# Performance work log

Hardware: AMD Instinct MI355X
Metric: run time of the kernel (lower is better)

The kernel has to match this reference:

```python
import jax, jax.numpy as jnp
import numpy as np

VEC_SIZE = 256
N_VECS = 8
N_CHOICES = 2048
BATCH = 2048
EPS = 1e-6
NAND_BIAS = 3.0


def setup_inputs() -> dict:
    key = jax.random.key(0)
    k1, k2 = jax.random.split(key)
    query = jax.random.normal(k1, (BATCH, N_VECS * VEC_SIZE), dtype=jnp.float32)
    weight = jax.random.normal(k2, (N_CHOICES, VEC_SIZE * N_VECS), dtype=jnp.float32)
    # init code overwrites the randn nand_weight with ones + nand_bias
    nand_weight = jnp.full((N_CHOICES, N_VECS), 1.0 + NAND_BIAS, dtype=jnp.float32)
    return {"query": query, "weight": weight, "nand_weight": nand_weight}


def reference(query, weight, nand_weight):
    # [B, n_vecs, vec_size] and [C, n_vecs, vec_size]
    q = query.reshape(-1, N_VECS, VEC_SIZE)
    w = weight.reshape(-1, N_VECS, VEC_SIZE)
    # torch.cosine_similarity clamps each norm to eps
    qn = q / jnp.maximum(jnp.linalg.norm(q, axis=-1, keepdims=True), EPS)
    wn = w / jnp.maximum(jnp.linalg.norm(w, axis=-1, keepdims=True), EPS)
    # broadcast cosine sim expressed as batched matmul: [B, C, n_vecs]
    cos_sim = jnp.einsum('bnd,cnd->bcn', qn, wn)
    cos_sim = jax.nn.leaky_relu(cos_sim)  # slope 0.01, matches F.leaky_relu default
    nw = jax.nn.sigmoid(nand_weight)[None]  # [1, C, n_vecs]
    interpolated = nw * cos_sim + (1.0 - nw) * (1.0 - cos_sim)
    return jnp.prod(interpolated, axis=2)  # [B, C]
```

## Files before the change

### kernel.cpp

```cpp
#include <hip/hip_runtime.h>
#include <math.h>
#include <stdint.h>

#define BATCH    2048
#define NCHOICES 2048
#define NV       8
#define VS       256
#define KTOT     2048

typedef unsigned short u16;
typedef __attribute__((ext_vector_type(8))) short    bf16x8;
typedef __attribute__((ext_vector_type(8))) u16      u16x8;
typedef __attribute__((ext_vector_type(4))) float    f32x4;

__device__ __forceinline__ u16 f2bf_rne(float x) {
    unsigned u = __float_as_uint(x);
    return (u16)((u + 0x7FFFu + ((u >> 16) & 1u)) >> 16);
}

__global__ __launch_bounds__(256) void prep_convert(
    const float* __restrict__ Q, const float* __restrict__ W,
    const float* __restrict__ NWT,
    u16* __restrict__ Qh, u16* __restrict__ Ql,
    u16* __restrict__ Wh, u16* __restrict__ Wl,
    float* __restrict__ rq, float* __restrict__ rw, float* __restrict__ snw)
{
    const int row = blockIdx.x;
    const int t   = threadIdx.x;
    const int n   = t >> 5;
    const int l   = t & 31;

    const float* src; u16 *dh, *dl; float* dst;
    if (row < BATCH) {
        src = Q + (size_t)row * KTOT;
        dh = Qh + (size_t)row * KTOT; dl = Ql + (size_t)row * KTOT;
        dst = rq + (size_t)row * NV;
    } else {
        src = W + (size_t)(row - BATCH) * KTOT;
        dh = Wh + (size_t)(row - BATCH) * KTOT; dl = Wl + (size_t)(row - BATCH) * KTOT;
        dst = rw + (size_t)(row - BATCH) * NV;
    }

    const int idx = n * VS + l * 8;
    float4 x0 = *(const float4*)(src + idx);
    float4 x1 = *(const float4*)(src + idx + 4);
    float xs[8] = {x0.x, x0.y, x0.z, x0.w, x1.x, x1.y, x1.z, x1.w};

    u16x8 hv, lv;
    float s = 0.0f;
    #pragma unroll
    for (int j = 0; j < 8; ++j) {
        u16 h = f2bf_rne(xs[j]);
        float hf = __uint_as_float(((unsigned)h) << 16);
        hv[j] = h;
        lv[j] = f2bf_rne(xs[j] - hf);
        s = fmaf(xs[j], xs[j], s);
    }
    *(u16x8*)(dh + idx) = hv;
    *(u16x8*)(dl + idx) = lv;

    #pragma unroll
    for (int m = 1; m < 32; m <<= 1) s += __shfl_xor(s, m, 64);
    if (l == 0) dst[n] = 1.0f / fmaxf(sqrtf(s), 1e-6f);

    if (row >= BATCH && t < NV) {
        const int c = row - BATCH;
        float x = NWT[(size_t)c * NV + t];
        snw[(size_t)c * NV + t] = 1.0f / (1.0f + expf(-x));
    }
}

__device__ __forceinline__ void gload16(const void* g, void* l) {
    __builtin_amdgcn_global_load_lds(
        (__attribute__((address_space(1))) void*)(uintptr_t)g,
        (__attribute__((address_space(3))) void*)(uint32_t)(uintptr_t)l,
        16, 0, 0);
}

__device__ __forceinline__ bf16x8 lds_rd16(const u16* p) {
    f32x4 r;
    asm volatile("ds_read_b128 %0, %1"
                 : "=v"(r)
                 : "v"((uint32_t)(uintptr_t)p));
    return __builtin_bit_cast(bf16x8, r);
}

#define SWZ(R, G) ((R) * 32 + ((((G) ^ (((R) >> 1) & 3))) << 3))

__global__ __launch_bounds__(512, 2) void nand_mfma8(
    const u16* __restrict__ Qh, const u16* __restrict__ Ql,
    const u16* __restrict__ Wh, const u16* __restrict__ Wl,
    const float* __restrict__ rq, const float* __restrict__ rw,
    const float* __restrict__ snw, float* __restrict__ part)
{
    __shared__ __align__(16) u16 L[3][24576];

    const int tid  = threadIdx.x;
    const int lane = tid & 63;
    const int wave = tid >> 6;
    const int wr   = (wave >> 2) * 64;
    const int wc   = (wave & 3) * 64;
    const int bm0  = blockIdx.y * 128;
    const int bn0  = blockIdx.x * 256;
    const int z    = blockIdx.z;
    const int kb   = z * 1024;

    const int fr = lane & 15;
    const int gi = lane >> 4;
    const int ri = gi * 4;

    const int gr  = tid >> 2;
    const int gg  = tid & 3;
    const int gsw = (gg ^ ((gr >> 1) & 3)) * 8;

    const u16* sAh  = Qh + (size_t)(bm0 + gr) * KTOT + kb + gsw;
    const u16* sAl  = Ql + (size_t)(bm0 + gr) * KTOT + kb + gsw;
    const u16* sB0h = Wh + (size_t)(bn0 + gr) * KTOT + kb + gsw;
    const u16* sB1h = Wh + (size_t)(bn0 + 128 + gr) * KTOT + kb + gsw;
    const u16* sB0l = Wl + (size_t)(bn0 + gr) * KTOT + kb + gsw;
    const u16* sB1l = Wl + (size_t)(bn0 + 128 + gr) * KTOT + kb + gsw;

    #define STAGE_A(B, T)  do { u16* Lb_ = &L[B][0];                        \
        gload16(sAh  + (T) * 32, Lb_ + tid * 8);                            \
        gload16(sAl  + (T) * 32, Lb_ + 4096  + tid * 8); } while (0)
    #define STAGE_BH(B, T) do { u16* Lb_ = &L[B][0];                        \
        gload16(sB0h + (T) * 32, Lb_ + 8192  + tid * 8);                    \
        gload16(sB1h + (T) * 32, Lb_ + 12288 + tid * 8); } while (0)
    #define STAGE_BL(B, T) do { u16* Lb_ = &L[B][0];                        \
        gload16(sB0l + (T) * 32, Lb_ + 16384 + tid * 8);                    \
        gload16(sB1l + (T) * 32, Lb_ + 20480 + tid * 8); } while (0)

    #define RD_A(M) do {                                                    \
        ah[M] = lds_rd16(Lb + SWZ(wr + (M) * 16 + fr, gi));                 \
        al[M] = lds_rd16(Lb + 4096 + SWZ(wr + (M) * 16 + fr, gi)); } while (0)
    #define RD_B(N) do {                                                    \
        bh[N] = lds_rd16(Lb + 8192  + SWZ(wc + (N) * 16 + fr, gi));         \
        bl[N] = lds_rd16(Lb + 16384 + SWZ(wc + (N) * 16 + fr, gi)); } while (0)

    #define MM(M, N) do {                                                   \
        acc[M][N] = __builtin_amdgcn_mfma_f32_16x16x32_bf16(ah[M], bh[N], acc[M][N], 0, 0, 0); \
        acc[M][N] = __builtin_amdgcn_mfma_f32_16x16x32_bf16(ah[M], bl[N], acc[M][N], 0, 0, 0); \
        acc[M][N] = __builtin_amdgcn_mfma_f32_16x16x32_bf16(al[M], bh[N], acc[M][N], 0, 0, 0); } while (0)

    #define WAIT_LGKM0() do {                                               \
        asm volatile("s_waitcnt lgkmcnt(0)");                               \
        __builtin_amdgcn_sched_barrier(0); } while (0)

    f32x4 prod[4][4];
    #pragma unroll
    for (int m = 0; m < 4; ++m)
        #pragma unroll
        for (int n = 0; n < 4; ++n) prod[m][n] = (f32x4){1.f, 1.f, 1.f, 1.f};

    STAGE_A(0, 0); STAGE_BH(0, 0); STAGE_BL(0, 0);
    STAGE_A(1, 1); STAGE_BH(1, 1); STAGE_BL(1, 1);
    asm volatile("s_waitcnt vmcnt(6)");
    __builtin_amdgcn_s_barrier();

    int buf = 0, bufp = 2;

    #pragma unroll 1
    for (int cc = 0; cc < 4; ++cc) {
        const int chunk = z * 4 + cc;

        float rqv[4][4];
        #pragma unroll
        for (int m = 0; m < 4; ++m)
            #pragma unroll
            for (int i = 0; i < 4; ++i)
                rqv[m][i] = rq[(size_t)(bm0 + wr + m * 16 + ri + i) * NV + chunk];
        float rwv[4], vv[4], uu[4];
        #pragma unroll
        for (int n = 0; n < 4; ++n) {
            const int col = bn0 + wc + n * 16 + fr;
            rwv[n] = rw[(size_t)col * NV + chunk];
            float s = snw[(size_t)col * NV + chunk];
            vv[n] = 2.0f * s - 1.0f;
            uu[n] = 1.0f - s;
        }

        f32x4 acc[4][4];
        #pragma unroll
        for (int m = 0; m < 4; ++m)
            #pragma unroll
            for (int n = 0; n < 4; ++n) acc[m][n] = (f32x4){0.f, 0.f, 0.f, 0.f};

        #pragma unroll 1
        for (int t8 = 0; t8 < 8; ++t8) {
            const int t = cc * 8 + t8;
            const u16* Lb = &L[buf][0];
            const bool pf = (t + 2) < 32;

            bf16x8 ah[4], al[4], bh[4], bl[4];

            RD_A(0); RD_A(1); RD_B(0); RD_B(1);
            if (pf) STAGE_A(bufp, t + 2);
            __builtin_amdgcn_s_barrier();
            WAIT_LGKM0();
            __builtin_amdgcn_s_setprio(1);
            MM(0, 0); MM(0, 1); MM(1, 0); MM(1, 1);
            __builtin_amdgcn_s_setprio(0);
            __builtin_amdgcn_s_barrier();

            RD_B(2); RD_B(3);
            if (pf) STAGE_BH(bufp, t + 2);
            __builtin_amdgcn_s_barrier();
            WAIT_LGKM0();
            __builtin_amdgcn_s_setprio(1);
            MM(0, 2); MM(0, 3); MM(1, 2); MM(1, 3);
            __builtin_amdgcn_s_setprio(0);
            __builtin_amdgcn_s_barrier();

            RD_A(2); RD_A(3);
            if (pf) STAGE_BL(bufp, t + 2);
            __builtin_amdgcn_s_barrier();
            WAIT_LGKM0();
            __builtin_amdgcn_s_setprio(1);
            MM(2, 2); MM(2, 3); MM(3, 2); MM(3, 3);
            __builtin_amdgcn_s_setprio(0);
            __builtin_amdgcn_s_barrier();

            __builtin_amdgcn_s_setprio(1);
            MM(2, 0); MM(2, 1); MM(3, 0); MM(3, 1);
            __builtin_amdgcn_s_setprio(0);

            if (t < 30) {
                asm volatile("s_waitcnt vmcnt(6)");
                __builtin_amdgcn_s_barrier();
            } else if (t == 30) {
                asm volatile("s_waitcnt vmcnt(0)");
                __builtin_amdgcn_s_barrier();
            }
            buf  = (buf  == 2) ? 0 : buf  + 1;
            bufp = (bufp == 2) ? 0 : bufp + 1;
        }

        #pragma unroll
        for (int m = 0; m < 4; ++m)
            #pragma unroll
            for (int i = 0; i < 4; ++i)
                #pragma unroll
                for (int n = 0; n < 4; ++n) {
                    float cosv = acc[m][n][i] * rqv[m][i] * rwv[n];
                    float Lk = fmaxf(cosv, 0.01f * cosv);
                    prod[m][n][i] *= fmaf(Lk, vv[n], uu[n]);
                }
    }

    float* P = part + (size_t)z * BATCH * NCHOICES;
    #pragma unroll
    for (int m = 0; m < 4; ++m)
        #pragma unroll
        for (int i = 0; i < 4; ++i) {
            const int row = bm0 + wr + m * 16 + ri + i;
            float* pr = P + (size_t)row * NCHOICES + bn0 + wc + fr;
            #pragma unroll
            for (int n = 0; n < 4; ++n) pr[n * 16] = prod[m][n][i];
        }

    #undef STAGE_A
    #undef STAGE_BH
    #undef STAGE_BL
    #undef RD_A
    #undef RD_B
    #undef MM
    #undef WAIT_LGKM0
}

__global__ __launch_bounds__(256) void combine_kernel(
    const float* __restrict__ p, float* __restrict__ out)
{
    const size_t NN = (size_t)BATCH * NCHOICES;
    size_t i = ((size_t)blockIdx.x * 256 + threadIdx.x) * 4;
    float4 a = *(const float4*)(p + i);
    float4 b = *(const float4*)(p + NN + i);
    float4 o;
    o.x = a.x * b.x;
    o.y = a.y * b.y;
    o.z = a.z * b.z;
    o.w = a.w * b.w;
    *(float4*)(out + i) = o;
}

__global__ __launch_bounds__(256) void prep_kernel(
    const float* __restrict__ Q, const float* __restrict__ W,
    const float* __restrict__ NWT,
    float* __restrict__ rq, float* __restrict__ rw, float* __restrict__ snw)
{
    const int row = blockIdx.x;
    const int t   = threadIdx.x;
    const int n   = t >> 5;
    const int l   = t & 31;

    const float* src; float* dst;
    if (row < BATCH) { src = Q + (size_t)row * KTOT; dst = rq + (size_t)row * NV; }
    else { src = W + (size_t)(row - BATCH) * KTOT; dst = rw + (size_t)(row - BATCH) * NV; }

    const float* v = src + n * VS + l * 8;
    float4 a = *(const float4*)(v);
    float4 b = *(const float4*)(v + 4);
    float s = a.x*a.x + a.y*a.y + a.z*a.z + a.w*a.w
            + b.x*b.x + b.y*b.y + b.z*b.z + b.w*b.w;
    #pragma unroll
    for (int m = 1; m < 32; m <<= 1) s += __shfl_xor(s, m, 64);
    if (l == 0) dst[n] = 1.0f / fmaxf(sqrtf(s), 1e-6f);
    if (row >= BATCH && t < NV) {
        const int c = row - BATCH;
        float x = NWT[(size_t)c * NV + t];
        snw[(size_t)c * NV + t] = 1.0f / (1.0f + expf(-x));
    }
}

__global__ __launch_bounds__(256, 2) void nand_gemm(
    const float* __restrict__ Q, const float* __restrict__ W,
    const float* __restrict__ rq, const float* __restrict__ rw,
    const float* __restrict__ snw, float* __restrict__ out)
{
    __shared__ __align__(16) float As[16][128 + 4];
    __shared__ __align__(16) float Bs[16][128 + 4];
    __shared__ __align__(16) float rqs[128];
    __shared__ __align__(16) float rws[128];
    __shared__ __align__(16) float sns[128];

    const int tid = threadIdx.x;
    const int tx  = tid & 15;
    const int ty  = tid >> 4;
    const int bm0 = blockIdx.y * 128;
    const int bn0 = blockIdx.x * 128;
    const int lr  = tid >> 2;
    const int lk  = (tid & 3) * 4;

    float prod[8][8];
    #pragma unroll
    for (int i = 0; i < 8; ++i)
        #pragma unroll
        for (int j = 0; j < 8; ++j) prod[i][j] = 1.0f;

    for (int n = 0; n < NV; ++n) {
        float acc[8][8];
        #pragma unroll
        for (int i = 0; i < 8; ++i)
            #pragma unroll
            for (int j = 0; j < 8; ++j) acc[i][j] = 0.0f;

        #pragma unroll 1
        for (int kt = 0; kt < VS / 16; ++kt) {
            const int k0 = n * VS + kt * 16;
            __syncthreads();
            {
                const float* qrow = Q + (size_t)(bm0 + lr) * KTOT + k0 + lk;
                float4 a0 = *(const float4*)(qrow);
                float4 a1 = *(const float4*)(qrow + (size_t)64 * KTOT);
                As[lk + 0][lr] = a0.x; As[lk + 1][lr] = a0.y;
                As[lk + 2][lr] = a0.z; As[lk + 3][lr] = a0.w;
                As[lk + 0][64 + lr] = a1.x; As[lk + 1][64 + lr] = a1.y;
                As[lk + 2][64 + lr] = a1.z; As[lk + 3][64 + lr] = a1.w;

                const float* wrow = W + (size_t)(bn0 + lr) * KTOT + k0 + lk;
                float4 b0 = *(const float4*)(wrow);
                float4 b1 = *(const float4*)(wrow + (size_t)64 * KTOT);
                Bs[lk + 0][lr] = b0.x; Bs[lk + 1][lr] = b0.y;
                Bs[lk + 2][lr] = b0.z; Bs[lk + 3][lr] = b0.w;
                Bs[lk + 0][64 + lr] = b1.x; Bs[lk + 1][64 + lr] = b1.y;
                Bs[lk + 2][64 + lr] = b1.z; Bs[lk + 3][64 + lr] = b1.w;
            }
            if (kt == 0) {
                for (int i = tid; i < 3 * 128; i += 256) {
                    if (i < 128)      rqs[i]       = rq[(size_t)(bm0 + i) * NV + n];
                    else if (i < 256) rws[i - 128] = rw[(size_t)(bn0 + i - 128) * NV + n];
                    else              sns[i - 256] = snw[(size_t)(bn0 + i - 256) * NV + n];
                }
            }
            __syncthreads();

            #pragma unroll
            for (int kk = 0; kk < 16; ++kk) {
                float4 a0 = *(const float4*)&As[kk][ty * 4];
                float4 a1 = *(const float4*)&As[kk][64 + ty * 4];
                float4 b0 = *(const float4*)&Bs[kk][tx * 4];
                float4 b1 = *(const float4*)&Bs[kk][64 + tx * 4];
                float ar[8] = {a0.x, a0.y, a0.z, a0.w, a1.x, a1.y, a1.z, a1.w};
                float br[8] = {b0.x, b0.y, b0.z, b0.w, b1.x, b1.y, b1.z, b1.w};
                #pragma unroll
                for (int i = 0; i < 8; ++i)
                    #pragma unroll
                    for (int j = 0; j < 8; ++j)
                        acc[i][j] = fmaf(ar[i], br[j], acc[i][j]);
            }
        }

        float rwv[8], uu[8], vv[8];
        #pragma unroll
        for (int j = 0; j < 8; ++j) {
            int cc = (j < 4) ? (tx * 4 + j) : (64 + tx * 4 + (j - 4));
            rwv[j] = rws[cc];
            float s = sns[cc];
            uu[j] = 1.0f - s;
            vv[j] = 2.0f * s - 1.0f;
        }
        #pragma unroll
        for (int i = 0; i < 8; ++i) {
            int r = (i < 4) ? (ty * 4 + i) : (64 + ty * 4 + (i - 4));
            float rqv = rqs[r];
            #pragma unroll
            for (int j = 0; j < 8; ++j) {
                float cosv = acc[i][j] * rqv * rwv[j];
                float Lk = fmaxf(cosv, 0.01f * cosv);
                prod[i][j] *= fmaf(Lk, vv[j], uu[j]);
            }
        }
    }

    #pragma unroll
    for (int i = 0; i < 8; ++i) {
        int r = (i < 4) ? (ty * 4 + i) : (64 + ty * 4 + (i - 4));
        float* orow = out + (size_t)(bm0 + r) * NCHOICES + bn0;
        float4 o0 = {prod[i][0], prod[i][1], prod[i][2], prod[i][3]};
        float4 o1 = {prod[i][4], prod[i][5], prod[i][6], prod[i][7]};
        *(float4*)(orow + tx * 4)      = o0;
        *(float4*)(orow + 64 + tx * 4) = o1;
    }
}

extern "C" void kernel_launch(void* const* d_in, const int* in_sizes, int n_in,
                              void* d_out, int out_size, void* d_ws, size_t ws_size,
                              hipStream_t stream)
{
    const float* Q   = (const float*)d_in[0];
    const float* W   = (const float*)d_in[1];
    const float* NWT = (const float*)d_in[2];
    float* out = (float*)d_out;

    char* w = (char*)d_ws;
    float* rq  = (float*)w; w += (size_t)BATCH    * NV * 4;
    float* rwn = (float*)w; w += (size_t)NCHOICES * NV * 4;
    float* snw = (float*)w; w += (size_t)NCHOICES * NV * 4;
    u16* Qh = (u16*)w; w += (size_t)BATCH * KTOT * 2;
    u16* Ql = (u16*)w; w += (size_t)BATCH * KTOT * 2;
    u16* Wh = (u16*)w; w += (size_t)NCHOICES * KTOT * 2;
    u16* Wl = (u16*)w; w += (size_t)NCHOICES * KTOT * 2;
    float* part = (float*)w; w += (size_t)2 * BATCH * NCHOICES * 4;
    const size_t needed = (size_t)(w - (char*)d_ws);

    if (ws_size >= needed) {
        prep_convert<<<BATCH + NCHOICES, 256, 0, stream>>>(
            Q, W, NWT, Qh, Ql, Wh, Wl, rq, rwn, snw);
        dim3 grid(NCHOICES / 256, BATCH / 128, 2);
        nand_mfma8<<<grid, 512, 0, stream>>>(Qh, Ql, Wh, Wl, rq, rwn, snw, part);
        combine_kernel<<<(BATCH * NCHOICES / 4) / 256, 256, 0, stream>>>(part, out);
    } else {
        prep_kernel<<<BATCH + NCHOICES, 256, 0, stream>>>(Q, W, NWT, rq, rwn, snw);
        dim3 grid(NCHOICES / 128, BATCH / 128);
        nand_gemm<<<grid, 256, 0, stream>>>(Q, W, rq, rwn, snw, out);
    }
}
```

Before: 84.51 us.

## Replace 8-wave triple-buffered GEMM with 4-wave double-buffered 128x128 tile kernel

The split-bf16 MFMA kernel goes from a 128x256 tile with 8 waves and a three-stage LDS ring to a 128x128 tile with 4 waves and a simple double buffer. Each step prefetches the next tile, reads all fragments, and issues all MFMAs in one block, with one barrier per step. The goal is to cut the many per-step barriers and the interleaving of phases, and to raise block count for better occupancy. In exchange, per-block data reuse drops (more global/L2 traffic per flop) and latency hiding is shallower.

```diff
diff --git a/kernel.cpp b/kernel.cpp
--- a/kernel.cpp
+++ b/kernel.cpp
@@ -87,21 +87,21 @@
 
 #define SWZ(R, G) ((R) * 32 + ((((G) ^ (((R) >> 1) & 3))) << 3))
 
-__global__ __launch_bounds__(512, 2) void nand_mfma8(
+__global__ __launch_bounds__(256, 2) void nand_mfma2b(
     const u16* __restrict__ Qh, const u16* __restrict__ Ql,
     const u16* __restrict__ Wh, const u16* __restrict__ Wl,
     const float* __restrict__ rq, const float* __restrict__ rw,
     const float* __restrict__ snw, float* __restrict__ part)
 {
-    __shared__ __align__(16) u16 L[3][24576];
+    __shared__ __align__(16) u16 L[2][16384];
 
     const int tid  = threadIdx.x;
     const int lane = tid & 63;
     const int wave = tid >> 6;
-    const int wr   = (wave >> 2) * 64;
-    const int wc   = (wave & 3) * 64;
+    const int wr   = (wave >> 1) * 64;
+    const int wc   = (wave & 1) * 64;
     const int bm0  = blockIdx.y * 128;
-    const int bn0  = blockIdx.x * 256;
+    const int bn0  = blockIdx.x * 128;
     const int z    = blockIdx.z;
     const int kb   = z * 1024;
 
@@ -109,66 +109,90 @@
     const int gi = lane >> 4;
     const int ri = gi * 4;
 
-    const int gr  = tid >> 2;
-    const int gg  = tid & 3;
-    const int gsw = (gg ^ ((gr >> 1) & 3)) * 8;
-
-    const u16* sAh  = Qh + (size_t)(bm0 + gr) * KTOT + kb + gsw;
-    const u16* sAl  = Ql + (size_t)(bm0 + gr) * KTOT + kb + gsw;
-    const u16* sB0h = Wh + (size_t)(bn0 + gr) * KTOT + kb + gsw;
-    const u16* sB1h = Wh + (size_t)(bn0 + 128 + gr) * KTOT + kb + gsw;
-    const u16* sB0l = Wl + (size_t)(bn0 + gr) * KTOT + kb + gsw;
-    const u16* sB1l = Wl + (size_t)(bn0 + 128 + gr) * KTOT + kb + gsw;
-
-    #define STAGE_A(B, T)  do { u16* Lb_ = &L[B][0];                        \
-        gload16(sAh  + (T) * 32, Lb_ + tid * 8);                            \
-        gload16(sAl  + (T) * 32, Lb_ + 4096  + tid * 8); } while (0)
-    #define STAGE_BH(B, T) do { u16* Lb_ = &L[B][0];                        \
-        gload16(sB0h + (T) * 32, Lb_ + 8192  + tid * 8);                    \
-        gload16(sB1h + (T) * 32, Lb_ + 12288 + tid * 8); } while (0)
-    #define STAGE_BL(B, T) do { u16* Lb_ = &L[B][0];                        \
-        gload16(sB0l + (T) * 32, Lb_ + 16384 + tid * 8);                    \
-        gload16(sB1l + (T) * 32, Lb_ + 20480 + tid * 8); } while (0)
+    const int lr = lane >> 2;
+    const int sw = 8 * ((lane & 3) ^ ((lane >> 3) & 3));
+    const int r0 = wave * 32 + lr;
+    const int r1 = r0 + 16;
+
+    const u16* sAh0 = Qh + (size_t)(bm0 + r0) * KTOT + kb + sw;
+    const u16* sAh1 = Qh + (size_t)(bm0 + r1) * KTOT + kb + sw;
+    const u16* sAl0 = Ql + (size_t)(bm0 + r0) * KTOT + kb + sw;
+    const u16* sAl1 = Ql + (size_t)(bm0 + r1) * KTOT + kb + sw;
+    const u16* sBh0 = Wh + (size_t)(bn0 + r0) * KTOT + kb + sw;
+    const u16* sBh1 = Wh + (size_t)(bn0 + r1) * KTOT + kb + sw;
+    const u16* sBl0 = Wl + (size_t)(bn0 + r0) * KTOT + kb + sw;
+    const u16* sBl1 = Wl + (size_t)(bn0 + r1) * KTOT + kb + sw;
+
+    #define STAGE(B, T) do { u16* Lb_ = &L[B][0]; const int ko = (T) * 32;   \
+        gload16(sAh0 + ko, Lb_ + wave * 1024);                               \
+        gload16(sAh1 + ko, Lb_ + wave * 1024 + 512);                         \
+        gload16(sAl0 + ko, Lb_ + 4096  + wave * 1024);                       \
+        gload16(sAl1 + ko, Lb_ + 4096  + wave * 1024 + 512);                 \
+        gload16(sBh0 + ko, Lb_ + 8192  + wave * 1024);                       \
+        gload16(sBh1 + ko, Lb_ + 8192  + wave * 1024 + 512);                 \
+        gload16(sBl0 + ko, Lb_ + 12288 + wave * 1024);                       \
+        gload16(sBl1 + ko, Lb_ + 12288 + wave * 1024 + 512);                 \
+    } while (0)
 
     #define RD_A(M) do {                                                    \
-        ah[M] = lds_rd16(Lb + SWZ(wr + (M) * 16 + fr, gi));                 \
+        ah[M] = lds_rd16(Lb + SWZ(wr + (M) * 16 + fr, gi));                  \
         al[M] = lds_rd16(Lb + 4096 + SWZ(wr + (M) * 16 + fr, gi)); } while (0)
     #define RD_B(N) do {                                                    \
-        bh[N] = lds_rd16(Lb + 8192  + SWZ(wc + (N) * 16 + fr, gi));         \
-        bl[N] = lds_rd16(Lb + 16384 + SWZ(wc + (N) * 16 + fr, gi)); } while (0)
+        bh[N] = lds_rd16(Lb + 8192  + SWZ(wc + (N) * 16 + fr, gi));          \
+        bl[N] = lds_rd16(Lb + 12288 + SWZ(wc + (N) * 16 + fr, gi)); } while (0)
 
     #define MM(M, N) do {                                                   \
         acc[M][N] = __builtin_amdgcn_mfma_f32_16x16x32_bf16(ah[M], bh[N], acc[M][N], 0, 0, 0); \
         acc[M][N] = __builtin_amdgcn_mfma_f32_16x16x32_bf16(ah[M], bl[N], acc[M][N], 0, 0, 0); \
         acc[M][N] = __builtin_amdgcn_mfma_f32_16x16x32_bf16(al[M], bh[N], acc[M][N], 0, 0, 0); } while (0)
 
-    #define WAIT_LGKM0() do {                                               \
-        asm volatile("s_waitcnt lgkmcnt(0)");                               \
-        __builtin_amdgcn_sched_barrier(0); } while (0)
-
     f32x4 prod[4][4];
     #pragma unroll
     for (int m = 0; m < 4; ++m)
         #pragma unroll
         for (int n = 0; n < 4; ++n) prod[m][n] = (f32x4){1.f, 1.f, 1.f, 1.f};
 
-    STAGE_A(0, 0); STAGE_BH(0, 0); STAGE_BL(0, 0);
-    STAGE_A(1, 1); STAGE_BH(1, 1); STAGE_BL(1, 1);
-    asm volatile("s_waitcnt vmcnt(6)");
+    STAGE(0, 0);
+    asm volatile("s_waitcnt vmcnt(0)");
     __builtin_amdgcn_s_barrier();
 
-    int buf = 0, bufp = 2;
+    int buf = 0;
 
     #pragma unroll 1
     for (int cc = 0; cc < 4; ++cc) {
         const int chunk = z * 4 + cc;
 
-        float rqv[4][4];
+        f32x4 acc[4][4];
         #pragma unroll
         for (int m = 0; m < 4; ++m)
             #pragma unroll
-            for (int i = 0; i < 4; ++i)
-                rqv[m][i] = rq[(size_t)(bm0 + wr + m * 16 + ri + i) * NV + chunk];
+            for (int n = 0; n < 4; ++n) acc[m][n] = (f32x4){0.f, 0.f, 0.f, 0.f};
+
+        #pragma unroll 1
+        for (int t8 = 0; t8 < 8; ++t8) {
+            const int t = cc * 8 + t8;
+            const u16* Lb = &L[buf][0];
+
+            if (t + 1 < 32) STAGE(buf ^ 1, t + 1);
+
+            bf16x8 ah[4], al[4], bh[4], bl[4];
+            RD_A(0); RD_A(1); RD_A(2); RD_A(3);
+            RD_B(0); RD_B(1); RD_B(2); RD_B(3);
+            asm volatile("s_waitcnt lgkmcnt(0)");
+            __builtin_amdgcn_sched_barrier(0);
+
+            __builtin_amdgcn_s_setprio(1);
+            MM(0, 0); MM(0, 1); MM(1, 0); MM(1, 1);
+            MM(0, 2); MM(0, 3); MM(1, 2); MM(1, 3);
+            MM(2, 2); MM(2, 3); MM(3, 2); MM(3, 3);
+            MM(2, 0); MM(2, 1); MM(3, 0); MM(3, 1);
+            __builtin_amdgcn_s_setprio(0);
+
+            asm volatile("s_waitcnt vmcnt(0)");
+            __builtin_amdgcn_s_barrier();
+            buf ^= 1;
+        }
+
         float rwv[4], vv[4], uu[4];
         #pragma unroll
         for (int n = 0; n < 4; ++n) {
@@ -178,73 +202,20 @@
             vv[n] = 2.0f * s - 1.0f;
             uu[n] = 1.0f - s;
         }
-
-        f32x4 acc[4][4];
-        #pragma unroll
-        for (int m = 0; m < 4; ++m)
-            #pragma unroll
-            for (int n = 0; n < 4; ++n) acc[m][n] = (f32x4){0.f, 0.f, 0.f, 0.f};
-
-        #pragma unroll 1
-        for (int t8 = 0; t8 < 8; ++t8) {
-            const int t = cc * 8 + t8;
-            const u16* Lb = &L[buf][0];
-            const bool pf = (t + 2) < 32;
-
-            bf16x8 ah[4], al[4], bh[4], bl[4];
-
-            RD_A(0); RD_A(1); RD_B(0); RD_B(1);
-            if (pf) STAGE_A(bufp, t + 2);
-            __builtin_amdgcn_s_barrier();
-            WAIT_LGKM0();
-            __builtin_amdgcn_s_setprio(1);
-            MM(0, 0); MM(0, 1); MM(1, 0); MM(1, 1);
-            __builtin_amdgcn_s_setprio(0);
-            __builtin_amdgcn_s_barrier();
-
-            RD_B(2); RD_B(3);
-            if (pf) STAGE_BH(bufp, t + 2);
-            __builtin_amdgcn_s_barrier();
-            WAIT_LGKM0();
-            __builtin_amdgcn_s_setprio(1);
-            MM(0, 2); MM(0, 3); MM(1, 2); MM(1, 3);
-            __builtin_amdgcn_s_setprio(0);
-            __builtin_amdgcn_s_barrier();
-
-            RD_A(2); RD_A(3);
-            if (pf) STAGE_BL(bufp, t + 2);
-            __builtin_amdgcn_s_barrier();
-            WAIT_LGKM0();
-            __builtin_amdgcn_s_setprio(1);
-            MM(2, 2); MM(2, 3); MM(3, 2); MM(3, 3);
-            __builtin_amdgcn_s_setprio(0);
-            __builtin_amdgcn_s_barrier();
-
-            __builtin_amdgcn_s_setprio(1);
-            MM(2, 0); MM(2, 1); MM(3, 0); MM(3, 1);
-            __builtin_amdgcn_s_setprio(0);
-
-            if (t < 30) {
-                asm volatile("s_waitcnt vmcnt(6)");
-                __builtin_amdgcn_s_barrier();
-            } else if (t == 30) {
-                asm volatile("s_waitcnt vmcnt(0)");
-                __builtin_amdgcn_s_barrier();
-            }
-            buf  = (buf  == 2) ? 0 : buf  + 1;
-            bufp = (bufp == 2) ? 0 : bufp + 1;
-        }
-
-        #pragma unroll
-        for (int m = 0; m < 4; ++m)
-            #pragma unroll
-            for (int i = 0; i < 4; ++i)
+        #pragma unroll
+        for (int m = 0; m < 4; ++m) {
+            #pragma unroll
+            for (int i = 0; i < 4; ++i) {
+                const float rqv =
+                    rq[(size_t)(bm0 + wr + m * 16 + ri + i) * NV + chunk];
                 #pragma unroll
                 for (int n = 0; n < 4; ++n) {
-                    float cosv = acc[m][n][i] * rqv[m][i] * rwv[n];
+                    float cosv = acc[m][n][i] * rqv * rwv[n];
                     float Lk = fmaxf(cosv, 0.01f * cosv);
                     prod[m][n][i] *= fmaf(Lk, vv[n], uu[n]);
                 }
+            }
+        }
     }
 
     float* P = part + (size_t)z * BATCH * NCHOICES;
@@ -258,13 +229,10 @@
             for (int n = 0; n < 4; ++n) pr[n * 16] = prod[m][n][i];
         }
 
-    #undef STAGE_A
-    #undef STAGE_BH
-    #undef STAGE_BL
+    #undef STAGE
     #undef RD_A
     #undef RD_B
     #undef MM
-    #undef WAIT_LGKM0
 }
 
 __global__ __launch_bounds__(256) void combine_kernel(
@@ -445,8 +413,8 @@
     if (ws_size >= needed) {
         prep_convert<<<BATCH + NCHOICES, 256, 0, stream>>>(
             Q, W, NWT, Qh, Ql, Wh, Wl, rq, rwn, snw);
-        dim3 grid(NCHOICES / 256, BATCH / 128, 2);
-        nand_mfma8<<<grid, 512, 0, stream>>>(Qh, Ql, Wh, Wl, rq, rwn, snw, part);
+        dim3 grid(NCHOICES / 128, BATCH / 128, 2);
+        nand_mfma2b<<<grid, 256, 0, stream>>>(Qh, Ql, Wh, Wl, rq, rwn, snw, part);
         combine_kernel<<<(BATCH * NCHOICES / 4) / 256, 256, 0, stream>>>(part, out);
     } else {
         prep_kernel<<<BATCH + NCHOICES, 256, 0, stream>>>(Q, W, NWT, rq, rwn, snw);
```

Result: no change. 83.24 us (-1.5%).
